# Kernel optimization log

Measured on AMD Instinct MI355X. Metric: run time of the kernel, lower is better.

The kernel has to match this reference:

```python
import jax, jax.numpy as jnp
import numpy as np

# Locally-connected 2D convolution (torch legacy SpatialConvolutionLocal)
# out[b,o,h,w] = sum_{c,i,j} weight[h,w,o,c,i,j] * x_pad[b,c,h*dH+i,w*dW+j] + bias[o,h,w]

B, CIN, IH, IW = 32, 32, 64, 64
COUT, KH, KW = 64, 3, 3
DH, DW = 1, 1
PADH, PADW = 1, 1
OH = (IH + 2 * PADH - KH) // DH + 1
OW = (IW + 2 * PADW - KW) // DW + 1


def setup_inputs() -> dict:
    key = jax.random.key(0)
    k1, k2, k3 = jax.random.split(key, 3)
    stdv = 1.0 / np.sqrt(KW * KH * CIN)
    x = jax.random.normal(k1, (B, CIN, IH, IW), dtype=jnp.float32)
    weight = jax.random.uniform(k2, (OH, OW, COUT, CIN, KH, KW), dtype=jnp.float32,
                                minval=-stdv, maxval=stdv)
    bias = jax.random.uniform(k3, (COUT, OH, OW), dtype=jnp.float32,
                              minval=-stdv, maxval=stdv)
    return {"x": x, "weight": weight, "bias": bias}


def _extract_patches(x):
    # x: [B, C, IH, IW] -> patches [B, C, KH, KW, OH, OW]
    xp = jnp.pad(x, ((0, 0), (0, 0), (PADH, PADH), (PADW, PADW)))
    rows = []
    for i in range(KH):  # small fixed kernel loop (9 iters), not a data-dim loop
        cols = []
        for j in range(KW):
            cols.append(xp[:, :, i:i + OH * DH:DH, j:j + OW * DW:DW])
        rows.append(jnp.stack(cols, axis=2))  # [B, C, KW, OH, OW]
    return jnp.stack(rows, axis=2)  # [B, C, KH, KW, OH, OW]


def reference(x, weight, bias):
    patches = _extract_patches(x)  # [B, C, KH, KW, OH, OW]
    # per-position GEMM: distinct weight matrix at each (h, w)
    out = jnp.einsum('bcijhw,hwocij->bohw', patches, weight)
    return out + bias[None]  # [B, COUT, OH, OW]
```

## Files before the change

### kernel.cpp

```cpp
#include <hip/hip_runtime.h>


typedef __attribute__((ext_vector_type(8))) short short8;
typedef __attribute__((ext_vector_type(16))) float f32x16;
typedef __attribute__((ext_vector_type(4))) float f32x4;

__device__ __forceinline__ unsigned f2bf(float f) {
    unsigned u = __builtin_bit_cast(unsigned, f);
    return (u + 0x7FFFu + ((u >> 16) & 1u)) >> 16;
}

__global__ __launch_bounds__(256, 4) void lcconv_kernel(
    const float* __restrict__ xg,
    const float* __restrict__ wg,
    const float* __restrict__ bg,
    float* __restrict__ outg)
{
    __shared__ unsigned short Xl[32 * 32 * 3 * 6];

    const int tid  = threadIdx.x;
    const int B    = blockIdx.x;
    const int xcd  = B & 7;
    const int slot = B >> 3;
    const int wm   = slot & 7;
    const int gi   = xcd * 32 + (slot >> 3);
    const int h    = gi >> 2;
    const int wq2  = (gi >> 1) & 1;
    const int oh   = gi & 1;
    const int w0   = wq2 * 32 + wm * 4;
    const int og   = oh * 32;

#pragma unroll
    for (int t = 0; t < 12; t++) {
        int task = t * 256 + tid;
        int b   = task / 96;
        int rem = task - b * 96;
        int c   = rem / 3;
        int y3  = rem - c * 3;
        int y   = h + y3 - 1;
        float v0 = 0.f, v1 = 0.f, v2 = 0.f, v3 = 0.f, v4 = 0.f, v5 = 0.f;
        if ((unsigned)y < 64u) {
            const float* row = xg + ((b * 32 + c) * 64 + y) * 64;
            float4 m = *(const float4*)(row + w0);
            v1 = m.x; v2 = m.y; v3 = m.z; v4 = m.w;
            if (w0 > 0)      v0 = row[w0 - 1];
            if (w0 + 4 < 64) v5 = row[w0 + 4];
        }
        int cr = (c + b) & 31;
        unsigned* dst = (unsigned*)(Xl + ((b * 32 + cr) * 3 + y3) * 6);
        dst[0] = f2bf(v0) | (f2bf(v1) << 16);
        dst[1] = f2bf(v2) | (f2bf(v3) << 16);
        dst[2] = f2bf(v4) | (f2bf(v5) << 16);
    }
    __syncthreads();

    const int lane = tid & 63;
    const int wv   = tid >> 6;
    const int n    = lane & 31;
    const int g    = lane >> 5;

    const float* wbase = wg
        + (((h * 64) + (w0 + wv)) * 64 + og + n) * 288 + g * 8;

    f32x16 acc;
#pragma unroll
    for (int i = 0; i < 16; i++) acc[i] = 0.f;

    const int abase = n * 576 + wv;

#pragma unroll
    for (int ks = 0; ks < 18; ks++) {
        f32x4 wa = __builtin_nontemporal_load((const f32x4*)(wbase + ks * 16));
        f32x4 wb = __builtin_nontemporal_load((const f32x4*)(wbase + ks * 16 + 4));

        short8 a;
        int k0 = ks * 16 + g * 8;
#pragma unroll
        for (int e = 0; e < 8; e++) {
            int k = k0 + e;
            int c = (k * 456) >> 12;
            int t = k - c * 9;
            int i = (t * 11) >> 5;
            int j = t - i * 3;
            int cr = (c + n) & 31;
            a[e] = (short)Xl[abase + cr * 18 + i * 6 + j];
        }

        short8 w8;
        w8[0] = (short)f2bf(wa[0]); w8[1] = (short)f2bf(wa[1]);
        w8[2] = (short)f2bf(wa[2]); w8[3] = (short)f2bf(wa[3]);
        w8[4] = (short)f2bf(wb[0]); w8[5] = (short)f2bf(wb[1]);
        w8[6] = (short)f2bf(wb[2]); w8[7] = (short)f2bf(wb[3]);

        acc = __builtin_amdgcn_mfma_f32_32x32x16_bf16(a, w8, acc, 0, 0, 0);
    }

    __syncthreads();
    float* outl = (float*)Xl;
#pragma unroll
    for (int r = 0; r < 16; r++) {
        int row = (r & 3) + 8 * (r >> 2) + 4 * g;
        outl[(wv * 32 + row) * 32 + n] = acc[r];
    }
    __syncthreads();

#pragma unroll
    for (int it = 0; it < 4; it++) {
        int id = it * 256 + tid;
        int b = id >> 5;
        int o = id & 31;
        float4 v;
        v.x = outl[0 * 1024 + b * 32 + o];
        v.y = outl[1 * 1024 + b * 32 + o];
        v.z = outl[2 * 1024 + b * 32 + o];
        v.w = outl[3 * 1024 + b * 32 + o];
        const float4 bb = *(const float4*)(bg + ((og + o) * 64 + h) * 64 + w0);
        v.x += bb.x; v.y += bb.y; v.z += bb.z; v.w += bb.w;
        *(float4*)(outg + ((b * 64 + og + o) * 64 + h) * 64 + w0) = v;
    }
}

extern "C" void kernel_launch(void* const* d_in, const int* in_sizes, int n_in,
                              void* d_out, int out_size, void* d_ws, size_t ws_size,
                              hipStream_t stream) {
    const float* x = (const float*)d_in[0];
    const float* w = (const float*)d_in[1];
    const float* b = (const float*)d_in[2];
    float* out = (float*)d_out;
    lcconv_kernel<<<dim3(2048), dim3(256), 0, stream>>>(x, w, b, out);
}
```

Baseline: 536.4 us.

## Stream weights into LDS via async global_load_lds with double buffering

Weight tiles now travel from global memory into a double-buffered LDS area through global_load_lds DMA instead of direct per-lane 32-byte register loads. Each k-step issues the next chunk's loads before waiting on the current one, and a swizzled layout keeps both the DMA writes and the reads conflict-free. The goal is better coalescing and overlap of the weight stream, which dominates traffic, with the MFMA work. In exchange LDS use rises by 16 KB and the occupancy hint drops from 4 to 3 blocks. Each wave waits on the load counter before reading its own slice, with no block-level barrier.

```diff
diff --git a/kernel.cpp b/kernel.cpp
--- a/kernel.cpp
+++ b/kernel.cpp
@@ -10,12 +10,19 @@
     return (u + 0x7FFFu + ((u >> 16) & 1u)) >> 16;
 }
 
-__global__ __launch_bounds__(256, 4) void lcconv_kernel(
+__device__ __forceinline__ void glds16(const float* g, float* l) {
+    __builtin_amdgcn_global_load_lds(
+        (const __attribute__((address_space(1))) void*)g,
+        (__attribute__((address_space(3))) void*)l, 16, 0, 0);
+}
+
+__global__ __launch_bounds__(256, 3) void lcconv_kernel(
     const float* __restrict__ xg,
     const float* __restrict__ wg,
     const float* __restrict__ bg,
     float* __restrict__ outg)
 {
+    __shared__ float Wb[2][2048];
     __shared__ unsigned short Xl[32 * 32 * 3 * 6];
 
     const int tid  = threadIdx.x;
@@ -29,6 +36,20 @@
     const int oh   = gi & 1;
     const int w0   = wq2 * 32 + wm * 4;
     const int og   = oh * 32;
+
+    const int lane = tid & 63;
+    const int wv   = tid >> 6;
+    const int n    = lane & 31;
+    const int g    = lane >> 5;
+
+    const int o0  = lane >> 2;
+    const int gsl = (lane & 3) ^ ((o0 >> 1) & 3);
+    const float* wrow = wg + ((h * 64 + w0 + wv) * 64 + og) * 288;
+    const float* sA = wrow + o0 * 288 + gsl * 4;
+    const float* sB = wrow + (16 + o0) * 288 + gsl * 4;
+
+    glds16(sA, &Wb[0][wv * 512]);
+    glds16(sB, &Wb[0][wv * 512 + 256]);
 
 #pragma unroll
     for (int t = 0; t < 12; t++) {
@@ -54,43 +75,45 @@
     }
     __syncthreads();
 
-    const int lane = tid & 63;
-    const int wv   = tid >> 6;
-    const int n    = lane & 31;
-    const int g    = lane >> 5;
-
-    const float* wbase = wg
-        + (((h * 64) + (w0 + wv)) * 64 + og + n) * 288 + g * 8;
-
     f32x16 acc;
 #pragma unroll
     for (int i = 0; i < 16; i++) acc[i] = 0.f;
 
+    const int srd   = (wv * 32 + n) * 16 + (((g << 1) ^ ((n >> 1) & 3)) << 2);
     const int abase = n * 576 + wv;
 
 #pragma unroll
-    for (int ks = 0; ks < 18; ks++) {
-        f32x4 wa = __builtin_nontemporal_load((const f32x4*)(wbase + ks * 16));
-        f32x4 wb = __builtin_nontemporal_load((const f32x4*)(wbase + ks * 16 + 4));
+    for (int c = 0; c < 18; c++) {
+        if (c < 17) {
+            glds16(sA + (c + 1) * 16, &Wb[(c + 1) & 1][wv * 512]);
+            glds16(sB + (c + 1) * 16, &Wb[(c + 1) & 1][wv * 512 + 256]);
+            asm volatile("s_waitcnt vmcnt(2)" ::: "memory");
+        } else {
+            asm volatile("s_waitcnt vmcnt(0)" ::: "memory");
+        }
+        __builtin_amdgcn_sched_barrier(0);
+
+        f32x4 wa  = *(const f32x4*)&Wb[c & 1][srd];
+        f32x4 wb4 = *(const f32x4*)&Wb[c & 1][srd ^ 4];
 
         short8 a;
-        int k0 = ks * 16 + g * 8;
+        int k0 = c * 16 + g * 8;
 #pragma unroll
         for (int e = 0; e < 8; e++) {
             int k = k0 + e;
-            int c = (k * 456) >> 12;
-            int t = k - c * 9;
+            int cc = (k * 456) >> 12;
+            int t = k - cc * 9;
             int i = (t * 11) >> 5;
             int j = t - i * 3;
-            int cr = (c + n) & 31;
+            int cr = (cc + n) & 31;
             a[e] = (short)Xl[abase + cr * 18 + i * 6 + j];
         }
 
         short8 w8;
-        w8[0] = (short)f2bf(wa[0]); w8[1] = (short)f2bf(wa[1]);
-        w8[2] = (short)f2bf(wa[2]); w8[3] = (short)f2bf(wa[3]);
-        w8[4] = (short)f2bf(wb[0]); w8[5] = (short)f2bf(wb[1]);
-        w8[6] = (short)f2bf(wb[2]); w8[7] = (short)f2bf(wb[3]);
+        w8[0] = (short)f2bf(wa[0]);  w8[1] = (short)f2bf(wa[1]);
+        w8[2] = (short)f2bf(wa[2]);  w8[3] = (short)f2bf(wa[3]);
+        w8[4] = (short)f2bf(wb4[0]); w8[5] = (short)f2bf(wb4[1]);
+        w8[6] = (short)f2bf(wb4[2]); w8[7] = (short)f2bf(wb4[3]);
 
         acc = __builtin_amdgcn_mfma_f32_32x32x16_bf16(a, w8, acc, 0, 0, 0);
     }
```

Measured after the change: 479.1 us. -10.7%, faster.

## Stream weights into LDS with double-buffered async loads and split-K across waves

Applied to the files above, without the earlier changes.

Weights are now staged into a large LDS ring with global_load_lds direct-to-LDS copies, double-buffered across eight phases so the next phase's weight tile loads while the current one is computed. The address pattern is XOR-swizzled. Each block now covers 4 output positions by all 64 output channels, halving the grid and reusing the input patch tile across both channel halves. Two waves split the K dimension and reduce through LDS. This trades occupancy (launch bounds 1, about 144KB of LDS) and only half the waves doing MFMA per phase for overlapping the weight stream, which is the dominant memory traffic.

```diff
diff --git a/kernel.cpp b/kernel.cpp
--- a/kernel.cpp
+++ b/kernel.cpp
@@ -10,25 +10,55 @@
     return (u + 0x7FFFu + ((u >> 16) & 1u)) >> 16;
 }
 
-__global__ __launch_bounds__(256, 4) void lcconv_kernel(
+__device__ __forceinline__ void glds16(const float* g, float* l) {
+    __builtin_amdgcn_global_load_lds(
+        (const __attribute__((address_space(1))) void*)g,
+        (__attribute__((address_space(3))) void*)l, 16, 0, 0);
+}
+
+__global__ __launch_bounds__(256, 1) void lcconv_kernel(
     const float* __restrict__ xg,
     const float* __restrict__ wg,
     const float* __restrict__ bg,
     float* __restrict__ outg)
 {
-    __shared__ unsigned short Xl[32 * 32 * 3 * 6];
+    __shared__ __align__(16) unsigned char Lds[147456];
+    float*          Wring = (float*)Lds;
+    unsigned short* Xl    = (unsigned short*)(Lds + 73728);
+    float*          Pred  = (float*)(Lds + 110592);
+    float*          outF  = (float*)(Lds + 114688);
+    (void)Wring;
 
-    const int tid  = threadIdx.x;
-    const int B    = blockIdx.x;
-    const int xcd  = B & 7;
-    const int slot = B >> 3;
-    const int wm   = slot & 7;
-    const int gi   = xcd * 32 + (slot >> 3);
-    const int h    = gi >> 2;
-    const int wq2  = (gi >> 1) & 1;
-    const int oh   = gi & 1;
-    const int w0   = wq2 * 32 + wm * 4;
-    const int og   = oh * 32;
+    const int tid = threadIdx.x;
+    const int Bq  = blockIdx.x;
+    const int xcd = Bq & 7;
+    const int idx = Bq >> 3;
+    const int h   = xcd * 8 + (idx >> 4);
+    const int w0  = (idx & 15) * 4;
+
+    const int lane = tid & 63;
+    const int wv   = tid >> 6;
+    const int n    = lane & 31;
+    const int g    = lane >> 5;
+    const int oh   = wv >> 1;
+    const int kh   = wv & 1;
+
+    int srcoff[9];
+#pragma unroll
+    for (int j = 0; j < 9; j++) {
+        int P  = wv * 576 + j * 64 + lane;
+        int rp = (P * 3641) >> 18;
+        int qp = P - rp * 72;
+        srcoff[j] = rp * 1152 + ((qp ^ (rp & 7)) << 4);
+    }
+
+    {
+        const char* rb = (const char*)(wg + ((h * 64 + w0) * 64) * 288);
+        float* db = (float*)(Lds + wv * 9216);
+#pragma unroll
+        for (int j = 0; j < 9; j++)
+            glds16((const float*)(rb + srcoff[j]), db + j * 256);
+    }
 
 #pragma unroll
     for (int t = 0; t < 12; t++) {
@@ -54,69 +84,94 @@
     }
     __syncthreads();
 
-    const int lane = tid & 63;
-    const int wv   = tid >> 6;
-    const int n    = lane & 31;
-    const int g    = lane >> 5;
-
-    const float* wbase = wg
-        + (((h * 64) + (w0 + wv)) * 64 + og + n) * 288 + g * 8;
-
     f32x16 acc;
 #pragma unroll
     for (int i = 0; i < 16; i++) acc[i] = 0.f;
 
-    const int abase = n * 576 + wv;
+    const int kh144  = kh * 144, kh36 = kh * 36;
+    const int g8     = g * 8,    g2   = g * 2;
+    const int nn1152 = n * 1152, n7   = n & 7;
 
+    for (int ph = 0; ph < 8; ph++) {
+        __syncthreads();
+
+        if (ph < 7) {
+            int p1 = ph + 1;
+            const char* rb = (const char*)(
+                wg + ((h * 64 + w0 + (p1 >> 1)) * 64 + (p1 & 1) * 32) * 288);
+            float* db = (float*)(Lds + (p1 & 1) * 36864 + wv * 9216);
 #pragma unroll
-    for (int ks = 0; ks < 18; ks++) {
-        f32x4 wa = __builtin_nontemporal_load((const f32x4*)(wbase + ks * 16));
-        f32x4 wb = __builtin_nontemporal_load((const f32x4*)(wbase + ks * 16 + 4));
-
-        short8 a;
-        int k0 = ks * 16 + g * 8;
-#pragma unroll
-        for (int e = 0; e < 8; e++) {
-            int k = k0 + e;
-            int c = (k * 456) >> 12;
-            int t = k - c * 9;
-            int i = (t * 11) >> 5;
-            int j = t - i * 3;
-            int cr = (c + n) & 31;
-            a[e] = (short)Xl[abase + cr * 18 + i * 6 + j];
+            for (int j = 0; j < 9; j++)
+                glds16((const float*)(rb + srcoff[j]), db + j * 256);
         }
 
-        short8 w8;
-        w8[0] = (short)f2bf(wa[0]); w8[1] = (short)f2bf(wa[1]);
-        w8[2] = (short)f2bf(wa[2]); w8[3] = (short)f2bf(wa[3]);
-        w8[4] = (short)f2bf(wb[0]); w8[5] = (short)f2bf(wb[1]);
-        w8[6] = (short)f2bf(wb[2]); w8[7] = (short)f2bf(wb[3]);
+        const int active = (oh == (ph & 1));
+        const int pos    = ph >> 1;
+        if (active) {
+            const char* Wt = (const char*)Lds + (ph & 1) * 36864;
+            const int   ab = n * 576 + pos;
+#pragma unroll
+            for (int s = 0; s < 9; s++) {
+                int q0 = kh36 + s * 4 + g2;
+                f32x4 wa = *(const f32x4*)(Wt + nn1152 + (((q0    ) ^ n7) << 4));
+                f32x4 wb = *(const f32x4*)(Wt + nn1152 + (((q0 + 1) ^ n7) << 4));
 
-        acc = __builtin_amdgcn_mfma_f32_32x32x16_bf16(a, w8, acc, 0, 0, 0);
-    }
+                short8 a;
+#pragma unroll
+                for (int e = 0; e < 8; e++) {
+                    int k  = kh144 + s * 16 + g8 + e;
+                    int c  = (k * 456) >> 12;
+                    int t2 = k - c * 9;
+                    int i  = (t2 * 11) >> 5;
+                    int j2 = t2 - i * 3;
+                    int cr = (c + n) & 31;
+                    a[e] = (short)Xl[ab + cr * 18 + i * 6 + j2];
+                }
 
-    __syncthreads();
-    float* outl = (float*)Xl;
+                short8 w8;
+                w8[0] = (short)f2bf(wa[0]); w8[1] = (short)f2bf(wa[1]);
+                w8[2] = (short)f2bf(wa[2]); w8[3] = (short)f2bf(wa[3]);
+                w8[4] = (short)f2bf(wb[0]); w8[5] = (short)f2bf(wb[1]);
+                w8[6] = (short)f2bf(wb[2]); w8[7] = (short)f2bf(wb[3]);
+
+                acc = __builtin_amdgcn_mfma_f32_32x32x16_bf16(a, w8, acc, 0, 0, 0);
+            }
+            if (kh == 0) {
 #pragma unroll
-    for (int r = 0; r < 16; r++) {
-        int row = (r & 3) + 8 * (r >> 2) + 4 * g;
-        outl[(wv * 32 + row) * 32 + n] = acc[r];
+                for (int r = 0; r < 16; r++) Pred[r * 64 + lane] = acc[r];
+            }
+        }
+        __syncthreads();
+
+        if (active && kh == 1) {
+#pragma unroll
+            for (int r = 0; r < 16; r++) {
+                float v = acc[r] + Pred[r * 64 + lane];
+                int b = (r & 3) + 8 * (r >> 2) + 4 * g;
+                outF[((oh * 4 + pos) * 32 + b) * 32 + n] = v;
+            }
+        }
+        if (active) {
+#pragma unroll
+            for (int i2 = 0; i2 < 16; i2++) acc[i2] = 0.f;
+        }
     }
     __syncthreads();
 
 #pragma unroll
-    for (int it = 0; it < 4; it++) {
+    for (int it = 0; it < 8; it++) {
         int id = it * 256 + tid;
-        int b = id >> 5;
-        int o = id & 31;
+        int b  = id >> 6;
+        int o  = id & 63;
+        const float* src = outF + (o >> 5) * 4096 + b * 32 + (o & 31);
         float4 v;
-        v.x = outl[0 * 1024 + b * 32 + o];
-        v.y = outl[1 * 1024 + b * 32 + o];
-        v.z = outl[2 * 1024 + b * 32 + o];
-        v.w = outl[3 * 1024 + b * 32 + o];
-        const float4 bb = *(const float4*)(bg + ((og + o) * 64 + h) * 64 + w0);
+        v.x = src[0];
+        v.y = src[1024];
+        v.z = src[2048];
+        v.w = src[3072];
+        const float4 bb = *(const float4*)(bg + (o * 64 + h) * 64 + w0);
         v.x += bb.x; v.y += bb.y; v.z += bb.z; v.w += bb.w;
-        *(float4*)(outg + ((b * 64 + og + o) * 64 + h) * 64 + w0) = v;
+        *(float4*)(outg + ((b * 64 + o) * 64 + h) * 64 + w0) = v;
     }
 }
 
@@ -127,5 +182,5 @@
     const float* w = (const float*)d_in[1];
     const float* b = (const float*)d_in[2];
     float* out = (float*)d_out;
-    lcconv_kernel<<<dim3(2048), dim3(256), 0, stream>>>(x, w, b, out);
+    lcconv_kernel<<<dim3(1024), dim3(256), 0, stream>>>(x, w, b, out);
 }
```

Measured after the change: 469.9 us. 1.14x faster.

## Stream weights via async global-to-LDS ring and pre-build im2col patches

Applied to the files above, without the earlier changes.

Weights are now streamed into a per-wave 5-slot LDS ring buffer with global_load_lds, prefetched 4 k-steps ahead, and synchronised with explicit vmcnt waits. The old approach issued direct nontemporal register loads per step. The input tile is laid out as a bf16 im2col patch matrix, so each MFMA A-fragment is a single vector LDS read instead of eight scattered reads with index math. Each block now covers 2 output columns by 64 output channels instead of 4 by 32, with the grid and occupancy (launch bounds 2) adjusted to match. The cost is much larger LDS use and lower occupancy.

```diff
diff --git a/kernel.cpp b/kernel.cpp
--- a/kernel.cpp
+++ b/kernel.cpp
@@ -10,113 +10,139 @@
     return (u + 0x7FFFu + ((u >> 16) & 1u)) >> 16;
 }
 
-__global__ __launch_bounds__(256, 4) void lcconv_kernel(
+__device__ __forceinline__ void glds16(const float* g, float* l) {
+    __builtin_amdgcn_global_load_lds(
+        (const __attribute__((address_space(1))) void*)g,
+        (__attribute__((address_space(3))) void*)l, 16, 0, 0);
+}
+
+#define P_STRIDE 312
+#define P_POS    (32 * P_STRIDE)
+#define RING_OFF 39936
+
+#define STEP(KS, VM)  do {                                                    \
+    if ((KS) + 4 < 18) {                                                      \
+        glds16(sA + ((KS) + 4) * 16, ringw + (((KS) + 4) % 5) * 512);         \
+        glds16(sB + ((KS) + 4) * 16, ringw + (((KS) + 4) % 5) * 512 + 256);   \
+    }                                                                         \
+    asm volatile("s_waitcnt vmcnt(" #VM ")" ::: "memory");                    \
+    __builtin_amdgcn_sched_barrier(0);                                        \
+    {                                                                         \
+        const char* wt = (const char*)(ringw + ((KS) % 5) * 512);             \
+        f32x4 wa = *(const f32x4*)(wt + rdA);                                 \
+        f32x4 wb = *(const f32x4*)(wt + rdB);                                 \
+        short8 pa = *(const short8*)(Pl16 + pbase + (KS) * 16);               \
+        short8 w8;                                                            \
+        w8[0] = (short)f2bf(wa[0]); w8[1] = (short)f2bf(wa[1]);               \
+        w8[2] = (short)f2bf(wa[2]); w8[3] = (short)f2bf(wa[3]);               \
+        w8[4] = (short)f2bf(wb[0]); w8[5] = (short)f2bf(wb[1]);               \
+        w8[6] = (short)f2bf(wb[2]); w8[7] = (short)f2bf(wb[3]);               \
+        acc = __builtin_amdgcn_mfma_f32_32x32x16_bf16(pa, w8, acc, 0, 0, 0);  \
+    }                                                                         \
+} while (0)
+
+__global__ __launch_bounds__(256, 2) void lcconv_kernel(
     const float* __restrict__ xg,
     const float* __restrict__ wg,
     const float* __restrict__ bg,
     float* __restrict__ outg)
 {
-    __shared__ unsigned short Xl[32 * 32 * 3 * 6];
+    __shared__ __align__(16) unsigned char Lds[80896];
+    unsigned short* Pl16 = (unsigned short*)Lds;
 
-    const int tid  = threadIdx.x;
-    const int B    = blockIdx.x;
-    const int xcd  = B & 7;
-    const int slot = B >> 3;
-    const int wm   = slot & 7;
-    const int gi   = xcd * 32 + (slot >> 3);
-    const int h    = gi >> 2;
-    const int wq2  = (gi >> 1) & 1;
-    const int oh   = gi & 1;
-    const int w0   = wq2 * 32 + wm * 4;
-    const int og   = oh * 32;
-
-#pragma unroll
-    for (int t = 0; t < 12; t++) {
-        int task = t * 256 + tid;
-        int b   = task / 96;
-        int rem = task - b * 96;
-        int c   = rem / 3;
-        int y3  = rem - c * 3;
-        int y   = h + y3 - 1;
-        float v0 = 0.f, v1 = 0.f, v2 = 0.f, v3 = 0.f, v4 = 0.f, v5 = 0.f;
-        if ((unsigned)y < 64u) {
-            const float* row = xg + ((b * 32 + c) * 64 + y) * 64;
-            float4 m = *(const float4*)(row + w0);
-            v1 = m.x; v2 = m.y; v3 = m.z; v4 = m.w;
-            if (w0 > 0)      v0 = row[w0 - 1];
-            if (w0 + 4 < 64) v5 = row[w0 + 4];
-        }
-        int cr = (c + b) & 31;
-        unsigned* dst = (unsigned*)(Xl + ((b * 32 + cr) * 3 + y3) * 6);
-        dst[0] = f2bf(v0) | (f2bf(v1) << 16);
-        dst[1] = f2bf(v2) | (f2bf(v3) << 16);
-        dst[2] = f2bf(v4) | (f2bf(v5) << 16);
-    }
-    __syncthreads();
+    const int tid = threadIdx.x;
+    const int B   = blockIdx.x;
+    const int xcd = B & 7;
+    const int idx = B >> 3;
+    const int h   = xcd * 8 + (idx >> 5);
+    const int w0  = (idx & 31) * 2;
 
     const int lane = tid & 63;
     const int wv   = tid >> 6;
     const int n    = lane & 31;
     const int g    = lane >> 5;
+    const int pos  = wv >> 1;
+    const int oh   = wv & 1;
 
-    const float* wbase = wg
-        + (((h * 64) + (w0 + wv)) * 64 + og + n) * 288 + g * 8;
+    float* ringw = (float*)(Lds + RING_OFF) + wv * 2560;
+
+    const float* wbase = wg + ((h * 64 + (w0 + pos)) * 64 + oh * 32) * 288;
+    const int rA = lane >> 2;
+    const int rB = 16 + rA;
+    const int qs = (lane & 3) ^ (rA & 3);
+    const float* sA = wbase + rA * 288 + qs * 4;
+    const float* sB = wbase + rB * 288 + qs * 4;
+
+    const int rdA = n * 64 + (((2 * g)     ^ (n & 3)) << 4);
+    const int rdB = n * 64 + (((2 * g + 1) ^ (n & 3)) << 4);
+    const int pbase = pos * P_POS + n * P_STRIDE + g * 8;
+
+#pragma unroll
+    for (int c0 = 0; c0 < 4; c0++) {
+        glds16(sA + c0 * 16, ringw + c0 * 512);
+        glds16(sB + c0 * 16, ringw + c0 * 512 + 256);
+    }
+
+    const int case2 = (w0 & 3) != 0;
+#pragma unroll
+    for (int t = 0; t < 12; t++) {
+        int task = t * 256 + tid;
+        int t3   = (task * 43691) >> 17;
+        int b = t3 >> 5, c = t3 & 31, y3 = task - t3 * 3;
+        int y = h + y3 - 1;
+        float c0 = 0.f, c1 = 0.f, c2 = 0.f, c3 = 0.f;
+        if ((unsigned)y < 64u) {
+            const float* row = xg + ((b * 32 + c) * 64 + y) * 64;
+            float4 m = *(const float4*)(row + (w0 & ~3));
+            if (!case2) {
+                c1 = m.x; c2 = m.y; c3 = m.z;
+                if (w0 > 0) c0 = row[w0 - 1];
+            } else {
+                c0 = m.y; c1 = m.z; c2 = m.w;
+                if (w0 + 2 < 64) c3 = row[w0 + 2];
+            }
+        }
+        int kb = c * 9 + y3 * 3;
+        unsigned short* p0 = Pl16 + b * P_STRIDE + kb;
+        unsigned short* p1 = p0 + P_POS;
+        unsigned short b0 = (unsigned short)f2bf(c0);
+        unsigned short b1 = (unsigned short)f2bf(c1);
+        unsigned short b2 = (unsigned short)f2bf(c2);
+        unsigned short b3 = (unsigned short)f2bf(c3);
+        p0[0] = b0; p0[1] = b1; p0[2] = b2;
+        p1[0] = b1; p1[1] = b2; p1[2] = b3;
+    }
+    __syncthreads();
 
     f32x16 acc;
 #pragma unroll
     for (int i = 0; i < 16; i++) acc[i] = 0.f;
 
-    const int abase = n * 576 + wv;
-
-#pragma unroll
-    for (int ks = 0; ks < 18; ks++) {
-        f32x4 wa = __builtin_nontemporal_load((const f32x4*)(wbase + ks * 16));
-        f32x4 wb = __builtin_nontemporal_load((const f32x4*)(wbase + ks * 16 + 4));
-
-        short8 a;
-        int k0 = ks * 16 + g * 8;
-#pragma unroll
-        for (int e = 0; e < 8; e++) {
-            int k = k0 + e;
-            int c = (k * 456) >> 12;
-            int t = k - c * 9;
-            int i = (t * 11) >> 5;
-            int j = t - i * 3;
-            int cr = (c + n) & 31;
-            a[e] = (short)Xl[abase + cr * 18 + i * 6 + j];
-        }
-
-        short8 w8;
-        w8[0] = (short)f2bf(wa[0]); w8[1] = (short)f2bf(wa[1]);
-        w8[2] = (short)f2bf(wa[2]); w8[3] = (short)f2bf(wa[3]);
-        w8[4] = (short)f2bf(wb[0]); w8[5] = (short)f2bf(wb[1]);
-        w8[6] = (short)f2bf(wb[2]); w8[7] = (short)f2bf(wb[3]);
-
-        acc = __builtin_amdgcn_mfma_f32_32x32x16_bf16(a, w8, acc, 0, 0, 0);
-    }
+    STEP(0, 8);  STEP(1, 8);  STEP(2, 8);  STEP(3, 8);
+    STEP(4, 8);  STEP(5, 8);  STEP(6, 8);  STEP(7, 8);
+    STEP(8, 8);  STEP(9, 8);  STEP(10, 8); STEP(11, 8);
+    STEP(12, 8); STEP(13, 8); STEP(14, 6); STEP(15, 4);
+    STEP(16, 2); STEP(17, 0);
 
     __syncthreads();
-    float* outl = (float*)Xl;
+    float* outF = (float*)(Lds + RING_OFF);
 #pragma unroll
     for (int r = 0; r < 16; r++) {
-        int row = (r & 3) + 8 * (r >> 2) + 4 * g;
-        outl[(wv * 32 + row) * 32 + n] = acc[r];
+        int b = (r & 3) + 8 * (r >> 2) + 4 * g;
+        outF[(pos * 32 + b) * 64 + oh * 32 + n] = acc[r];
     }
     __syncthreads();
 
 #pragma unroll
-    for (int it = 0; it < 4; it++) {
+    for (int it = 0; it < 8; it++) {
         int id = it * 256 + tid;
-        int b = id >> 5;
-        int o = id & 31;
-        float4 v;
-        v.x = outl[0 * 1024 + b * 32 + o];
-        v.y = outl[1 * 1024 + b * 32 + o];
-        v.z = outl[2 * 1024 + b * 32 + o];
-        v.w = outl[3 * 1024 + b * 32 + o];
-        const float4 bb = *(const float4*)(bg + ((og + o) * 64 + h) * 64 + w0);
-        v.x += bb.x; v.y += bb.y; v.z += bb.z; v.w += bb.w;
-        *(float4*)(outg + ((b * 64 + og + o) * 64 + h) * 64 + w0) = v;
+        int b = id >> 6, o = id & 63;
+        float2 v;
+        v.x = outF[b * 64 + o];
+        v.y = outF[2048 + b * 64 + o];
+        const float2 bb = *(const float2*)(bg + (o * 64 + h) * 64 + w0);
+        v.x += bb.x; v.y += bb.y;
+        *(float2*)(outg + ((b * 64 + o) * 64 + h) * 64 + w0) = v;
     }
 }
 
```

Measured after the change: 469.6 us. -12.5%, faster.
